# Kernel optimization log

Hardware: AMD Instinct MI355X
Metric: run time of the kernel (lower is better)

Reference implementation:

```python
import jax, jax.numpy as jnp
import numpy as np

N_NODES = 50000
N_EDGES = 800000
IN_CH = 256
OUT_CH = 128


def setup_inputs() -> dict:
    key = jax.random.key(0)
    k1, k2, k3, k4, k5, k6 = jax.random.split(key, 6)
    x = jax.random.normal(k1, (N_NODES, IN_CH), dtype=jnp.float32)
    edge_rows = jax.random.randint(k2, (N_EDGES,), 0, N_NODES, dtype=jnp.int64)
    edge_cols = jax.random.randint(k3, (N_EDGES,), 0, N_NODES, dtype=jnp.int64)
    # positive edge weights, roughly like a normalized adjacency (~1/degree)
    edge_vals = jax.random.uniform(k4, (N_EDGES,), dtype=jnp.float32) / 16.0
    # xavier_uniform: bound = sqrt(6/(fan_in+fan_out))
    bound = float(np.sqrt(6.0 / (IN_CH + OUT_CH)))
    weight = jax.random.uniform(k5, (IN_CH, OUT_CH), dtype=jnp.float32, minval=-bound, maxval=bound)
    gate_weight = jax.random.uniform(k6, (IN_CH, OUT_CH), dtype=jnp.float32, minval=-bound, maxval=bound)
    return {"x": x, "edge_rows": edge_rows, "edge_cols": edge_cols,
            "edge_vals": edge_vals, "weight": weight, "gate_weight": gate_weight}


def _spmm(edge_rows, edge_cols, edge_vals, dense, n_rows):
    # out[r] = sum over edges (r, c, v): v * dense[c]
    gathered = edge_vals[:, None] * dense[edge_cols]  # [E, out_ch]
    return jax.ops.segment_sum(gathered, edge_rows, num_segments=n_rows)


def reference(x, edge_rows, edge_cols, edge_vals, weight, gate_weight):
    support = x @ weight          # [N, out_ch]
    gate = x @ gate_weight        # [N, out_ch]
    n = x.shape[0]
    agg_support = _spmm(edge_rows, edge_cols, edge_vals, support, n)
    agg_gate = _spmm(edge_rows, edge_cols, edge_vals, gate, n)
    return jax.nn.sigmoid(agg_gate) * agg_support
```

## Files before the change

kernel.cpp:

```cpp
#include <hip/hip_runtime.h>
#include <hip/hip_bf16.h>

#define IN_CH 256
#define OUT_CH 128
#define NCAT 256
#define CAP 64
#define RPB 128
#define BINCAP 3072
#define EPB 4096

typedef __attribute__((ext_vector_type(8))) short bf16x8;
typedef __attribute__((ext_vector_type(4))) float f32x4;

__device__ __forceinline__ unsigned short f2bf(float f) {
  unsigned int u = __builtin_bit_cast(unsigned int, f);
  u += 0x7FFFu + ((u >> 16) & 1u);
  return (unsigned short)(u >> 16);
}
__device__ __forceinline__ unsigned int pack2bf(float a, float b) {
  return (unsigned int)f2bf(a) | ((unsigned int)f2bf(b) << 16);
}
__device__ __forceinline__ float bflo(unsigned int u) {
  return __builtin_bit_cast(float, u << 16);
}
__device__ __forceinline__ float bfhi(unsigned int u) {
  return __builtin_bit_cast(float, u & 0xFFFF0000u);
}

__global__ __launch_bounds__(256) void init_wcat(
    const float* __restrict__ w, const float* __restrict__ gw,
    unsigned short* __restrict__ wcatT, int* __restrict__ coarse_cnt,
    int nbins) {
  const int b = blockIdx.x;
  if (b < 256) {
    const int c = b;
    const int k = threadIdx.x;
    const float v = (c < 128) ? w[(size_t)k * 128 + c]
                              : gw[(size_t)k * 128 + (c - 128)];
    wcatT[(size_t)c * 256 + k] = f2bf(v);
  } else {
    for (int j = threadIdx.x; j < nbins; j += 256) coarse_cnt[j] = 0;
  }
}

#define BM 128
#define BK 64
#define LDSTRIDE 144

__global__ __launch_bounds__(512) void gemm_and_bin(
    const float* __restrict__ x, const unsigned short* __restrict__ wcatT,
    char* __restrict__ comb, int nrows,
    const int* __restrict__ er, const int* __restrict__ ec,
    const float* __restrict__ ev, int* __restrict__ coarse_cnt,
    unsigned* __restrict__ cA, unsigned char* __restrict__ cB,
    int E, int nbins, int binBlocks) {
  __shared__ char smem[55296];

  if (blockIdx.x < binBlocks) {
    int* scnt = (int*)smem;
    int* sbase = (int*)smem + 512;
    const int t = threadIdx.x;
    const int e0 = blockIdx.x * EPB;

    if (t < 512) scnt[t] = 0;
    __syncthreads();

    int myr[8];
#pragma unroll
    for (int i = 0; i < 8; ++i) {
      const int e = e0 + i * 512 + t;
      int r = -1;
      if (e < E) { r = er[e]; atomicAdd(&scnt[r >> 7], 1); }
      myr[i] = r;
    }
    __syncthreads();

    if (t < nbins)
      sbase[t] = (scnt[t] > 0) ? atomicAdd(&coarse_cnt[t], scnt[t]) : 0;
    __syncthreads();
    if (t < 512) scnt[t] = 0;
    __syncthreads();

#pragma unroll
    for (int i = 0; i < 8; ++i) {
      const int r = myr[i];
      if (r >= 0) {
        const int e = e0 + i * 512 + t;
        const int b = r >> 7;
        const int idx = sbase[b] + atomicAdd(&scnt[b], 1);
        if (idx < BINCAP) {
          const size_t g = (size_t)b * BINCAP + idx;
          cA[g] = ((unsigned)ec[e] << 16) | (unsigned)f2bf(ev[e]);
          cB[g] = (unsigned char)(r & (RPB - 1));
        }
      }
    }
    return;
  }

  char* As = smem;
  char* Bs = smem + 18432;

  const int t = threadIdx.x;
  const int lane = t & 63;
  const int wv = t >> 6;
  const int wr = wv >> 2;
  const int wc = wv & 3;
  const int blockRow = (blockIdx.x - binBlocks) * BM;
  const int lrow = lane & 15;
  const int klane = lane >> 4;

  f32x4 acc[4][4];
#pragma unroll
  for (int m = 0; m < 4; ++m)
#pragma unroll
    for (int n = 0; n < 4; ++n) acc[m][n] = (f32x4){0.f, 0.f, 0.f, 0.f};

  const int arow = t >> 2;
  const int aseg = t & 3;
  const int agrow = blockRow + arow;
  const bool aok = (agrow < nrows);
  const float* xrow = x + (size_t)agrow * IN_CH;

  const int bc = t >> 1;
  const int bhalf = t & 1;

  for (int kt = 0; kt < IN_CH; kt += BK) {
    {
      float4 v0 = make_float4(0, 0, 0, 0), v1 = v0, v2 = v0, v3 = v0;
      if (aok) {
        const float* p = xrow + kt + aseg * 16;
        v0 = *(const float4*)(p + 0);
        v1 = *(const float4*)(p + 4);
        v2 = *(const float4*)(p + 8);
        v3 = *(const float4*)(p + 12);
      }
      uint4 pk0, pk1;
      pk0.x = pack2bf(v0.x, v0.y); pk0.y = pack2bf(v0.z, v0.w);
      pk0.z = pack2bf(v1.x, v1.y); pk0.w = pack2bf(v1.z, v1.w);
      pk1.x = pack2bf(v2.x, v2.y); pk1.y = pack2bf(v2.z, v2.w);
      pk1.z = pack2bf(v3.x, v3.y); pk1.w = pack2bf(v3.z, v3.w);
      char* dst = As + arow * LDSTRIDE + aseg * 32;
      *(uint4*)(dst + 0)  = pk0;
      *(uint4*)(dst + 16) = pk1;
    }
    {
      const char* src = (const char*)wcatT + (size_t)bc * 512 + kt * 2 + bhalf * 64;
      char* dst = Bs + bc * LDSTRIDE + bhalf * 64;
#pragma unroll
      for (int j = 0; j < 4; ++j)
        *(uint4*)(dst + j * 16) = *(const uint4*)(src + j * 16);
    }
    __syncthreads();

#pragma unroll
    for (int kk = 0; kk < 2; ++kk) {
      bf16x8 af[4], bfm[4];
#pragma unroll
      for (int m = 0; m < 4; ++m)
        af[m] = *(const bf16x8*)(As + (wr * 64 + m * 16 + lrow) * LDSTRIDE + kk * 64 + klane * 16);
#pragma unroll
      for (int n = 0; n < 4; ++n)
        bfm[n] = *(const bf16x8*)(Bs + (wc * 64 + n * 16 + lrow) * LDSTRIDE + kk * 64 + klane * 16);
#pragma unroll
      for (int m = 0; m < 4; ++m)
#pragma unroll
        for (int n = 0; n < 4; ++n)
          acc[m][n] = __builtin_amdgcn_mfma_f32_16x16x32_bf16(af[m], bfm[n], acc[m][n], 0, 0, 0);
    }
    __syncthreads();
  }

#pragma unroll
  for (int h = 0; h < 2; ++h) {
    if (wr == h) {
#pragma unroll
      for (int m = 0; m < 4; ++m) {
#pragma unroll
        for (int n = 0; n < 4; ++n) {
#pragma unroll
          for (int j = 0; j < 4; ++j) {
            const int rl = m * 16 + klane * 4 + j;
            const int gcol = wc * 64 + n * 16 + lrow;
            const int ch = gcol & 127;
            const int isg = gcol >> 7;
            const int byteoff = (ch >> 1) * 8 + isg * 4 + (ch & 1) * 2;
            *(unsigned short*)(smem + rl * 512 + byteoff) = f2bf(acc[m][n][j]);
          }
        }
      }
    }
    __syncthreads();
#pragma unroll
    for (int it = 0; it < 4; ++it) {
      const int lin = it * 512 + t;
      const int rl = lin >> 5;
      const int grow = blockRow + h * 64 + rl;
      if (grow < nrows)
        *(float4*)(comb + (size_t)grow * 512 + (lin & 31) * 16) =
            *(const float4*)(smem + lin * 16);
    }
    __syncthreads();
  }
}

__global__ __launch_bounds__(256) void bin_fine(
    const int* __restrict__ coarse_cnt, const unsigned* __restrict__ cA,
    const unsigned char* __restrict__ cB, int* __restrict__ cnt,
    unsigned* __restrict__ bucket4, int nrows) {
  __shared__ unsigned fine[RPB * CAP];
  __shared__ int lcnt[RPB];
  const int t = threadIdx.x;
  const int b = blockIdx.x;
  const int r0 = b * RPB;

  for (int j = t; j < RPB; j += 256) lcnt[j] = 0;
  __syncthreads();

  const int nE = min(coarse_cnt[b], BINCAP);
  for (int i = t; i < nE; i += 256) {
    const unsigned a = cA[(size_t)b * BINCAP + i];
    const int rl = cB[(size_t)b * BINCAP + i];
    const int idx = atomicAdd(&lcnt[rl], 1);
    if (idx < CAP) fine[rl * CAP + idx] = a;
  }
  __syncthreads();

  if (t < RPB && r0 + t < nrows) cnt[r0 + t] = min(lcnt[t], CAP);

  for (int s = t; s < RPB * CAP; s += 256) {
    const int rl = s >> 6;
    const int sl = s & 63;
    if (sl < min(lcnt[rl], CAP) && r0 + rl < nrows)
      bucket4[(size_t)(r0 + rl) * CAP + sl] = fine[s];
  }
}

__global__ __launch_bounds__(256) void spmm_fused(
    const unsigned* __restrict__ bucket4, const int* __restrict__ cnt,
    const char* __restrict__ comb, float* __restrict__ out, int nrows) {
  const int wid = (int)((blockIdx.x * 256 + threadIdx.x) >> 6);
  const int lane = threadIdx.x & 63;
  if (wid >= nrows) return;

  const int deg = min(cnt[wid], CAP);
  float s0 = 0.f, s1 = 0.f, g0 = 0.f, g1 = 0.f;

  if (deg > 0) {
    const unsigned my = bucket4[(size_t)wid * CAP + lane];
    for (int d = 0; d < deg; d += 8) {
      unsigned cj[8]; float vj[8]; uint2 q[8];
#pragma unroll
      for (int j = 0; j < 8; ++j) {
        const int dj = d + j;
        const int ds = dj < deg ? dj : deg - 1;
        const unsigned ent = (unsigned)__shfl((int)my, ds);
        cj[j] = ent >> 16;
        vj[j] = (dj < deg) ? bflo(ent) : 0.f;
      }
#pragma unroll
      for (int j = 0; j < 8; ++j)
        q[j] = *(const uint2*)(comb + (size_t)cj[j] * 512 + lane * 8);
#pragma unroll
      for (int j = 0; j < 8; ++j) {
        s0 += vj[j] * bflo(q[j].x);  s1 += vj[j] * bfhi(q[j].x);
        g0 += vj[j] * bflo(q[j].y);  g1 += vj[j] * bfhi(q[j].y);
      }
    }
  }
  const float o0 = s0 / (1.f + __expf(-g0));
  const float o1 = s1 / (1.f + __expf(-g1));
  *(float2*)&out[(size_t)wid * OUT_CH + lane * 2] = make_float2(o0, o1);
}

extern "C" void kernel_launch(void* const* d_in, const int* in_sizes, int n_in,
                              void* d_out, int out_size, void* d_ws, size_t ws_size,
                              hipStream_t stream) {
  const float* x  = (const float*)d_in[0];
  const int*   er = (const int*)d_in[1];
  const int*   ec = (const int*)d_in[2];
  const float* ev = (const float*)d_in[3];
  const float* w  = (const float*)d_in[4];
  const float* gw = (const float*)d_in[5];
  float* out = (float*)d_out;

  const int N = in_sizes[0] / IN_CH;
  const int E = in_sizes[1];
  const int nbins = (N + RPB - 1) / RPB;

  char* ws = (char*)d_ws;
  char* comb = ws;
  size_t off = (size_t)N * 512;
  unsigned short* wcatT = (unsigned short*)(ws + off);  off += 256 * 256 * 2;
  int* cnt = (int*)(ws + off);                          off += ((size_t)N * 4 + 255) & ~255ull;
  unsigned* bucket4 = (unsigned*)(ws + off);            off += (size_t)N * CAP * 4;
  int* coarse_cnt = (int*)(ws + off);                   off += ((size_t)nbins * 4 + 255) & ~255ull;
  unsigned* cA = (unsigned*)(ws + off);                 off += (size_t)nbins * BINCAP * 4;
  unsigned char* cB = (unsigned char*)(ws + off);

  init_wcat<<<257, 256, 0, stream>>>(w, gw, wcatT, coarse_cnt, nbins);

  const int binBlocks = (E + EPB - 1) / EPB;
  const int gemmBlocks = (N + BM - 1) / BM;
  gemm_and_bin<<<binBlocks + gemmBlocks, 512, 0, stream>>>(
      x, wcatT, comb, N, er, ec, ev, coarse_cnt, cA, cB, E, nbins, binBlocks);

  bin_fine<<<nbins, 256, 0, stream>>>(coarse_cnt, cA, cB, cnt, bucket4, N);

  const int blocks = (N + 3) / 4;
  spmm_fused<<<blocks, 256, 0, stream>>>(bucket4, cnt, comb, out, N);
}
```

Baseline: 109.7 us.

## Stage full A tile in LDS once and read B fragments directly from global

The GEMM no longer loops over four K-tiles with paired syncs. It converts and stores the whole 128x256 A tile into LDS in one pass, then runs all eight MFMA k-steps back to back, loading B fragments straight from global/L2 into registers instead of staging them in LDS. This removes the repeated barriers and the B LDS round trip. In exchange it uses more LDS per block (about 66KB), which may lower occupancy, and the B reads come from global memory with less coalescing.

```diff
diff --git a/kernel.cpp b/kernel.cpp
--- a/kernel.cpp
+++ b/kernel.cpp
@@ -44,8 +44,7 @@
 }
 
 #define BM 128
-#define BK 64
-#define LDSTRIDE 144
+#define AST 528
 
 __global__ __launch_bounds__(512) void gemm_and_bin(
     const float* __restrict__ x, const unsigned short* __restrict__ wcatT,
@@ -54,7 +53,7 @@
     const float* __restrict__ ev, int* __restrict__ coarse_cnt,
     unsigned* __restrict__ cA, unsigned char* __restrict__ cB,
     int E, int nbins, int binBlocks) {
-  __shared__ char smem[55296];
+  __shared__ char smem[BM * AST];
 
   if (blockIdx.x < binBlocks) {
     int* scnt = (int*)smem;
@@ -98,9 +97,6 @@
     return;
   }
 
-  char* As = smem;
-  char* Bs = smem + 18432;
-
   const int t = threadIdx.x;
   const int lane = t & 63;
   const int wv = t >> 6;
@@ -110,66 +106,57 @@
   const int lrow = lane & 15;
   const int klane = lane >> 4;
 
-  f32x4 acc[4][4];
-#pragma unroll
-  for (int m = 0; m < 4; ++m)
-#pragma unroll
-    for (int n = 0; n < 4; ++n) acc[m][n] = (f32x4){0.f, 0.f, 0.f, 0.f};
-
-  const int arow = t >> 2;
-  const int aseg = t & 3;
-  const int agrow = blockRow + arow;
-  const bool aok = (agrow < nrows);
-  const float* xrow = x + (size_t)agrow * IN_CH;
-
-  const int bc = t >> 1;
-  const int bhalf = t & 1;
-
-  for (int kt = 0; kt < IN_CH; kt += BK) {
-    {
+  {
+    const int arow = t >> 2;
+    const int aseg = t & 3;
+    const int agrow = blockRow + arow;
+    const bool aok = (agrow < nrows);
+    const float* src = x + (size_t)agrow * IN_CH + aseg * 64;
+    char* dst = smem + arow * AST + aseg * 128;
+#pragma unroll
+    for (int g = 0; g < 4; ++g) {
       float4 v0 = make_float4(0, 0, 0, 0), v1 = v0, v2 = v0, v3 = v0;
       if (aok) {
-        const float* p = xrow + kt + aseg * 16;
-        v0 = *(const float4*)(p + 0);
-        v1 = *(const float4*)(p + 4);
-        v2 = *(const float4*)(p + 8);
-        v3 = *(const float4*)(p + 12);
+        v0 = *(const float4*)(src + g * 16 + 0);
+        v1 = *(const float4*)(src + g * 16 + 4);
+        v2 = *(const float4*)(src + g * 16 + 8);
+        v3 = *(const float4*)(src + g * 16 + 12);
       }
       uint4 pk0, pk1;
       pk0.x = pack2bf(v0.x, v0.y); pk0.y = pack2bf(v0.z, v0.w);
       pk0.z = pack2bf(v1.x, v1.y); pk0.w = pack2bf(v1.z, v1.w);
       pk1.x = pack2bf(v2.x, v2.y); pk1.y = pack2bf(v2.z, v2.w);
       pk1.z = pack2bf(v3.x, v3.y); pk1.w = pack2bf(v3.z, v3.w);
-      char* dst = As + arow * LDSTRIDE + aseg * 32;
-      *(uint4*)(dst + 0)  = pk0;
-      *(uint4*)(dst + 16) = pk1;
-    }
-    {
-      const char* src = (const char*)wcatT + (size_t)bc * 512 + kt * 2 + bhalf * 64;
-      char* dst = Bs + bc * LDSTRIDE + bhalf * 64;
-#pragma unroll
-      for (int j = 0; j < 4; ++j)
-        *(uint4*)(dst + j * 16) = *(const uint4*)(src + j * 16);
-    }
-    __syncthreads();
-
-#pragma unroll
-    for (int kk = 0; kk < 2; ++kk) {
-      bf16x8 af[4], bfm[4];
-#pragma unroll
-      for (int m = 0; m < 4; ++m)
-        af[m] = *(const bf16x8*)(As + (wr * 64 + m * 16 + lrow) * LDSTRIDE + kk * 64 + klane * 16);
+      *(uint4*)(dst + g * 32 + 0)  = pk0;
+      *(uint4*)(dst + g * 32 + 16) = pk1;
+    }
+  }
+  __syncthreads();
+
+  f32x4 acc[4][4];
+#pragma unroll
+  for (int m = 0; m < 4; ++m)
+#pragma unroll
+    for (int n = 0; n < 4; ++n) acc[m][n] = (f32x4){0.f, 0.f, 0.f, 0.f};
+
+  const char* bbase = (const char*)wcatT + (size_t)(wc * 64 + lrow) * 512 + klane * 16;
+
+#pragma unroll
+  for (int kk = 0; kk < 8; ++kk) {
+    bf16x8 af[4], bfr[4];
+#pragma unroll
+    for (int m = 0; m < 4; ++m)
+      af[m] = *(const bf16x8*)(smem + (wr * 64 + m * 16 + lrow) * AST + kk * 64 + klane * 16);
+#pragma unroll
+    for (int n = 0; n < 4; ++n)
+      bfr[n] = *(const bf16x8*)(bbase + (size_t)n * 16 * 512 + kk * 64);
+#pragma unroll
+    for (int m = 0; m < 4; ++m)
 #pragma unroll
       for (int n = 0; n < 4; ++n)
-        bfm[n] = *(const bf16x8*)(Bs + (wc * 64 + n * 16 + lrow) * LDSTRIDE + kk * 64 + klane * 16);
-#pragma unroll
-      for (int m = 0; m < 4; ++m)
-#pragma unroll
-        for (int n = 0; n < 4; ++n)
-          acc[m][n] = __builtin_amdgcn_mfma_f32_16x16x32_bf16(af[m], bfm[n], acc[m][n], 0, 0, 0);
-    }
-    __syncthreads();
-  }
+        acc[m][n] = __builtin_amdgcn_mfma_f32_16x16x32_bf16(af[m], bfr[n], acc[m][n], 0, 0, 0);
+  }
+  __syncthreads();
 
 #pragma unroll
   for (int h = 0; h < 2; ++h) {
```

After: 119.3 us. 8.7% more time.
